# Optimization experiments

Hardware: AMD Instinct MI355X
Metric: run time of the kernel (lower is better)

## Reference

```python
import jax, jax.numpy as jnp
import numpy as np
from jax.ops import segment_sum, segment_max

N, F, H, HEADS, E, OUT = 50000, 256, 64, 4, 800000, 16


def setup_inputs() -> dict:
    key = jax.random.key(0)
    ks = jax.random.split(key, 16)
    s = 0.05
    return {
        "x": jax.random.normal(ks[0], (N, F), jnp.float32),
        "edge_index": jax.random.randint(ks[1], (2, E), 0, N, jnp.int64),
        # GCN layer params
        "W_gcn1": jax.random.normal(ks[2], (F, H), jnp.float32) * s,
        "b_gcn1": jnp.zeros((H,), jnp.float32),
        "W_gcn2": jax.random.normal(ks[3], (H, OUT), jnp.float32) * s,
        "b_gcn2": jnp.zeros((OUT,), jnp.float32),
        # GAT layer 1 (heads=HEADS, concat)
        "W_gat1": jax.random.normal(ks[4], (F, HEADS * H), jnp.float32) * s,
        "a_src1": jax.random.normal(ks[5], (HEADS, H), jnp.float32) * s,
        "a_dst1": jax.random.normal(ks[6], (HEADS, H), jnp.float32) * s,
        "b_gat1": jnp.zeros((HEADS * H,), jnp.float32),
        # GAT layer 2 (heads=1, concat=False)
        "W_gat2": jax.random.normal(ks[7], (HEADS * H, OUT), jnp.float32) * s,
        "a_src2": jax.random.normal(ks[8], (1, OUT), jnp.float32) * s,
        "a_dst2": jax.random.normal(ks[9], (1, OUT), jnp.float32) * s,
        "b_gat2": jnp.zeros((OUT,), jnp.float32),
    }


def _add_self_loops(edge_index, n):
    loop = jnp.arange(n, dtype=edge_index.dtype)
    src = jnp.concatenate([edge_index[0], loop])
    dst = jnp.concatenate([edge_index[1], loop])
    return src, dst


def _gcn(x, src, dst, norm, W, b, n):
    h = x @ W  # [N, out]
    out = segment_sum(h[src] * norm[:, None], dst, num_segments=n)
    return out + b


def _gat(x, src, dst, W, a_s, a_d, b, heads, concat, n):
    h = (x @ W).reshape(n, heads, -1)  # [N, heads, C]
    s_src = jnp.einsum("nhc,hc->nh", h, a_s)
    s_dst = jnp.einsum("nhc,hc->nh", h, a_d)
    e = jax.nn.leaky_relu(s_src[src] + s_dst[dst], 0.2)  # [Etot, heads]
    m = segment_max(e, dst, num_segments=n)               # per-dst softmax
    p = jnp.exp(e - m[dst])
    denom = segment_sum(p, dst, num_segments=n)
    alpha = p / denom[dst]
    out = segment_sum(h[src] * alpha[..., None], dst, num_segments=n)
    out = out.reshape(n, -1) if concat else out.mean(axis=1)
    return out + b


def reference(x, edge_index, W_gcn1, b_gcn1, W_gcn2, b_gcn2,
              W_gat1, a_src1, a_dst1, b_gat1,
              W_gat2, a_src2, a_dst2, b_gat2):
    n = x.shape[0]
    src, dst = _add_self_loops(edge_index, n)
    # symmetric GCN normalization on self-loop-augmented graph
    deg = segment_sum(jnp.ones_like(dst, x.dtype), dst, num_segments=n)
    dinv = jnp.where(deg > 0, jax.lax.rsqrt(deg), 0.0)
    norm = dinv[src] * dinv[dst]

    x_gcn = jax.nn.relu(_gcn(x, src, dst, norm, W_gcn1, b_gcn1, n))
    x_gcn = _gcn(x_gcn, src, dst, norm, W_gcn2, b_gcn2, n)

    x_gat = jax.nn.relu(_gat(x, src, dst, W_gat1, a_src1, a_dst1, b_gat1, HEADS, True, n))
    x_gat = _gat(x_gat, src, dst, W_gat2, a_src2, a_dst2, b_gat2, 1, False, n)

    return jnp.concatenate([x_gcn, x_gat], axis=1)
```

## Files before the change

### kernel.cpp

```cpp
#include <hip/hip_runtime.h>
#include <math.h>

#define NN     50000
#define FF     256
#define HH     64
#define NHEADS 4
#define EE     800000
#define OUTD   16

typedef __attribute__((ext_vector_type(8))) short short8;
typedef __attribute__((ext_vector_type(4))) float f32x4;

__device__ inline unsigned short f2bf(float f) {
    unsigned u = __builtin_bit_cast(unsigned, f);
    unsigned r = (u + 0x7fff + ((u >> 16) & 1)) >> 16;
    return (unsigned short)r;
}
__device__ inline float bf2f(unsigned short s) {
    unsigned u = ((unsigned)s) << 16;
    return __builtin_bit_cast(float, u);
}

__global__ void k_zero_int(int* __restrict__ p, int n) {
    int i = blockIdx.x * blockDim.x + threadIdx.x;
    if (i < n) p[i] = 0;
}

__global__ void k_count(const int* __restrict__ dst, int* __restrict__ cnt, int e) {
    int i = blockIdx.x * blockDim.x + threadIdx.x;
    if (i < e) atomicAdd(&cnt[dst[i]], 1);
}

__global__ __launch_bounds__(256) void k_scan_a(const int* __restrict__ cnt,
                                                int* __restrict__ partial, int n) {
    int i = blockIdx.x * 256 + threadIdx.x;
    int v = (i < n) ? cnt[i] : 0;
#pragma unroll
    for (int off = 32; off >= 1; off >>= 1) v += __shfl_xor(v, off, 64);
    __shared__ int ws[4];
    int wave = threadIdx.x >> 6;
    if ((threadIdx.x & 63) == 0) ws[wave] = v;
    __syncthreads();
    if (threadIdx.x == 0) partial[blockIdx.x] = ws[0] + ws[1] + ws[2] + ws[3];
}

__global__ __launch_bounds__(256) void k_scan_b(const int* __restrict__ partial,
                                                int* __restrict__ blockoff,
                                                int* __restrict__ total_out, int nb) {
    __shared__ int arr[256];
    int tid = threadIdx.x;
    arr[tid] = (tid < nb) ? partial[tid] : 0;
    __syncthreads();
#pragma unroll
    for (int off = 1; off < 256; off <<= 1) {
        int v = arr[tid];
        int add = (tid >= off) ? arr[tid - off] : 0;
        __syncthreads();
        arr[tid] = v + add;
        __syncthreads();
    }
    if (tid < nb) blockoff[tid] = arr[tid] - partial[tid];
    if (tid == 0) *total_out = arr[255];
}

__global__ __launch_bounds__(256) void k_scan_c(const int* __restrict__ cnt,
                                                const int* __restrict__ blockoff,
                                                int* __restrict__ row_start,
                                                int* __restrict__ cursor,
                                                float* __restrict__ dinv, int n) {
    __shared__ int arr[256];
    int tid = threadIdx.x;
    int i = blockIdx.x * 256 + tid;
    int c = (i < n) ? cnt[i] : 0;
    arr[tid] = c;
    __syncthreads();
#pragma unroll
    for (int off = 1; off < 256; off <<= 1) {
        int v = arr[tid];
        int add = (tid >= off) ? arr[tid - off] : 0;
        __syncthreads();
        arr[tid] = v + add;
        __syncthreads();
    }
    if (i < n) {
        int excl = arr[tid] - c + blockoff[blockIdx.x];
        row_start[i] = excl;
        cursor[i] = excl;
        dinv[i] = rsqrtf((float)(c + 1));
    }
}

__global__ void k_fill(const int* __restrict__ src, const int* __restrict__ dst,
                       int* __restrict__ cursor, int* __restrict__ col, int e) {
    int i = blockIdx.x * blockDim.x + threadIdx.x;
    if (i < e) {
        int d = dst[i];
        int pos = atomicAdd(&cursor[d], 1);
        col[pos] = src[i];
    }
}

template <int KB, int NT>
__global__ void k_pack_w(const float* __restrict__ W,
                         unsigned short* __restrict__ bhi,
                         unsigned short* __restrict__ blo) {
    int t_ = blockIdx.x * blockDim.x + threadIdx.x;
    const int total = KB * NT * 64;
    if (t_ >= total) return;
    int lane = t_ & 63;
    int tile = (t_ >> 6) % NT;
    int kb = (t_ >> 6) / NT;
    int q = lane >> 4, c = lane & 15;
    const int NC = NT * 16;
    size_t off = ((size_t)(kb * NT + tile) * 64 + lane) * 8;
#pragma unroll
    for (int j = 0; j < 8; j++) {
        float w = W[(size_t)(kb * 32 + q * 8 + j) * NC + tile * 16 + c];
        unsigned short h = f2bf(w);
        bhi[off + j] = h;
        blo[off + j] = f2bf(w - bf2f(h));
    }
}

template <int NT, bool SCALE, bool SCORES>
__global__ __launch_bounds__(256) void mfma_gemm(const float* __restrict__ A,
                                                 const unsigned short* __restrict__ Bhi,
                                                 const unsigned short* __restrict__ Blo,
                                                 unsigned short* __restrict__ Cbf,
                                                 const float* __restrict__ rowscale,
                                                 const float* __restrict__ a_s,
                                                 const float* __restrict__ a_d,
                                                 float* __restrict__ ssrc,
                                                 float* __restrict__ sdst,
                                                 int M) {
    const int K = 256, NC = NT * 16;
    __shared__ short8 bsh[NT * 64];
    __shared__ short8 bsl[NT * 64];
    int tid = threadIdx.x;
    int w = tid >> 6, lane = tid & 63, q = lane >> 4, c = lane & 15;
    int row_base = blockIdx.x * 64 + w * 16;
    int ar = min(row_base + c, M - 1);
    const float* ap = A + (size_t)ar * K + q * 8;

    f32x4 acc[NT];
#pragma unroll
    for (int t = 0; t < NT; t++) acc[t] = (f32x4){0.f, 0.f, 0.f, 0.f};

    for (int kb = 0; kb < 8; kb++) {
        float av[8];
        *(float4*)(av)     = *(const float4*)(ap + kb * 32);
        *(float4*)(av + 4) = *(const float4*)(ap + kb * 32 + 4);
        short8 ahi, alo;
#pragma unroll
        for (int j = 0; j < 8; j++) {
            unsigned short h = f2bf(av[j]);
            ahi[j] = (short)h;
            alo[j] = (short)f2bf(av[j] - bf2f(h));
        }
        const short8* gh = (const short8*)(Bhi + (size_t)kb * NT * 512);
        const short8* gl = (const short8*)(Blo + (size_t)kb * NT * 512);
        __syncthreads();
        for (int i = tid; i < NT * 64; i += 256) {
            bsh[i] = gh[i];
            bsl[i] = gl[i];
        }
        __syncthreads();
#pragma unroll
        for (int t = 0; t < NT; t++) {
            short8 bhi = bsh[t * 64 + lane];
            short8 blo = bsl[t * 64 + lane];
            acc[t] = __builtin_amdgcn_mfma_f32_16x16x32_bf16(ahi, bhi, acc[t], 0, 0, 0);
            acc[t] = __builtin_amdgcn_mfma_f32_16x16x32_bf16(alo, bhi, acc[t], 0, 0, 0);
            acc[t] = __builtin_amdgcn_mfma_f32_16x16x32_bf16(ahi, blo, acc[t], 0, 0, 0);
        }
    }

    if (SCORES) {
#pragma unroll
        for (int i = 0; i < 4; i++) {
            int r = row_base + q * 4 + i;
            float ss[4] = {0.f, 0.f, 0.f, 0.f};
            float sd[4] = {0.f, 0.f, 0.f, 0.f};
#pragma unroll
            for (int t = 0; t < NT; t++) {
                float v = acc[t][i];
                ss[t >> 2] += v * a_s[t * 16 + c];
                sd[t >> 2] += v * a_d[t * 16 + c];
            }
#pragma unroll
            for (int h = 0; h < 4; h++) {
#pragma unroll
                for (int off = 1; off <= 8; off <<= 1) {
                    ss[h] += __shfl_xor(ss[h], off, 16);
                    sd[h] += __shfl_xor(sd[h], off, 16);
                }
            }
            if (c == i && r < M) {
                *(float4*)(ssrc + (size_t)r * 4) = make_float4(ss[0], ss[1], ss[2], ss[3]);
                *(float4*)(sdst + (size_t)r * 4) = make_float4(sd[0], sd[1], sd[2], sd[3]);
            }
        }
    }

#pragma unroll
    for (int i = 0; i < 4; i++) {
        int r = row_base + q * 4 + i;
        if (r < M) {
            float sc = SCALE ? rowscale[r] : 1.0f;
#pragma unroll
            for (int t = 0; t < NT; t++)
                Cbf[(size_t)r * NC + t * 16 + c] = f2bf(acc[t][i] * sc);
        }
    }
}

template <int KB, bool SCALE, bool SC2>
__global__ __launch_bounds__(256) void mfma_n16(const unsigned short* __restrict__ A,
                                                const unsigned short* __restrict__ Bhi,
                                                const unsigned short* __restrict__ Blo,
                                                unsigned short* __restrict__ Cbf,
                                                const float* __restrict__ rowscale,
                                                const float* __restrict__ a_s2,
                                                const float* __restrict__ a_d2,
                                                float* __restrict__ s2s,
                                                float* __restrict__ s2d, int M) {
    const int K = KB * 32;
    int tid = threadIdx.x;
    int w = tid >> 6, lane = tid & 63, q = lane >> 4, c = lane & 15;
    int row_base = blockIdx.x * 64 + w * 16;
    int ar = min(row_base + c, M - 1);
    const unsigned short* ap = A + (size_t)ar * K + q * 8;
    f32x4 acc = (f32x4){0.f, 0.f, 0.f, 0.f};
#pragma unroll
    for (int kb = 0; kb < KB; kb++) {
        short8 av = *(const short8*)(ap + kb * 32);
        size_t bo = ((size_t)kb * 64 + lane) * 8;
        short8 bh = *(const short8*)(Bhi + bo);
        short8 bl = *(const short8*)(Blo + bo);
        acc = __builtin_amdgcn_mfma_f32_16x16x32_bf16(av, bh, acc, 0, 0, 0);
        acc = __builtin_amdgcn_mfma_f32_16x16x32_bf16(av, bl, acc, 0, 0, 0);
    }
    if (SC2) {
#pragma unroll
        for (int i = 0; i < 4; i++) {
            float ps = acc[i] * a_s2[c];
            float pd = acc[i] * a_d2[c];
#pragma unroll
            for (int off = 1; off <= 8; off <<= 1) {
                ps += __shfl_xor(ps, off, 16);
                pd += __shfl_xor(pd, off, 16);
            }
            int r = row_base + q * 4 + i;
            if (c == i && r < M) {
                s2s[r] = ps;
                s2d[r] = pd;
            }
        }
    }
#pragma unroll
    for (int i = 0; i < 4; i++) {
        int r = row_base + q * 4 + i;
        if (r < M) {
            float sc = SCALE ? rowscale[r] : 1.0f;
            Cbf[(size_t)r * 16 + c] = f2bf(acc[i] * sc);
        }
    }
}

__global__ __launch_bounds__(256) void gcn1_agg(const unsigned short* __restrict__ h,
                                                const int* __restrict__ rs,
                                                const int* __restrict__ col,
                                                const float* __restrict__ dinv,
                                                const float* __restrict__ b,
                                                unsigned short* __restrict__ out) {
    int wid = (blockIdx.x * 256 + threadIdx.x) >> 6;
    int lane = threadIdx.x & 63;
    if (wid >= NN) return;
    int g = lane >> 4;
    int cidx = (lane & 15) * 4;
    float di = dinv[wid];
    int beg = rs[wid], end = rs[wid + 1];
    float4 acc = make_float4(0.f, 0.f, 0.f, 0.f);

    for (int j0 = beg; j0 < end; j0 += 64) {
        int cnt = min(64, end - j0);
        int sreg = 0;
        if (lane < cnt) sreg = col[j0 + lane];
        for (int e = 0; e < cnt; e += 8) {
            int myE0 = e + g, myE1 = e + g + 4;
            int s0 = __shfl(sreg, myE0, 64);
            int s1 = __shfl(sreg, myE1, 64);
            ushort4 v0 = make_ushort4(0, 0, 0, 0), v1 = make_ushort4(0, 0, 0, 0);
            if (myE0 < cnt) v0 = *(const ushort4*)(h + (size_t)s0 * HH + cidx);
            if (myE1 < cnt) v1 = *(const ushort4*)(h + (size_t)s1 * HH + cidx);
            acc.x += bf2f(v0.x) + bf2f(v1.x);
            acc.y += bf2f(v0.y) + bf2f(v1.y);
            acc.z += bf2f(v0.z) + bf2f(v1.z);
            acc.w += bf2f(v0.w) + bf2f(v1.w);
        }
    }
#pragma unroll
    for (int off = 16; off <= 32; off <<= 1) {
        acc.x += __shfl_xor(acc.x, off, 64);
        acc.y += __shfl_xor(acc.y, off, 64);
        acc.z += __shfl_xor(acc.z, off, 64);
        acc.w += __shfl_xor(acc.w, off, 64);
    }
    if (g == 0) {
        ushort4 sv = *(const ushort4*)(h + (size_t)wid * HH + cidx);
        float4 bv = *(const float4*)(b + cidx);
        ushort4 o;
        o.x = f2bf(fmaxf((acc.x + bf2f(sv.x)) * di + bv.x, 0.f));
        o.y = f2bf(fmaxf((acc.y + bf2f(sv.y)) * di + bv.y, 0.f));
        o.z = f2bf(fmaxf((acc.z + bf2f(sv.z)) * di + bv.z, 0.f));
        o.w = f2bf(fmaxf((acc.w + bf2f(sv.w)) * di + bv.w, 0.f));
        *(ushort4*)(out + (size_t)wid * HH + cidx) = o;
    }
}

__global__ __launch_bounds__(256) void gat1_agg(const unsigned short* __restrict__ hg,
                                                const int* __restrict__ rs,
                                                const int* __restrict__ col,
                                                const float* __restrict__ ssrc,
                                                const float* __restrict__ sdst,
                                                const float* __restrict__ b,
                                                unsigned short* __restrict__ out) {
    __shared__ int s_lds[4][64];
    __shared__ float p_lds[4][64 * 4];
    int tid = threadIdx.x;
    int w = tid >> 6, lane = tid & 63;
    int wid = blockIdx.x * 4 + w;
    int hh = lane >> 4;
    int* sl = s_lds[w];
    float* pl = p_lds[w];

    float4 sd4 = *(const float4*)(sdst + (size_t)wid * 4);
    float sdv[4] = {sd4.x, sd4.y, sd4.z, sd4.w};
    float4 sf4 = *(const float4*)(ssrc + (size_t)wid * 4);
    float sfv[4] = {sf4.x, sf4.y, sf4.z, sf4.w};
    float psf[4];
#pragma unroll
    for (int h = 0; h < 4; h++) {
        float e = sfv[h] + sdv[h];
        e = (e >= 0.f) ? e : 0.2f * e;
        psf[h] = __expf(e);
    }
    float pse = (hh & 2) ? ((hh & 1) ? psf[3] : psf[2]) : ((hh & 1) ? psf[1] : psf[0]);
    const unsigned short* hbase = hg + lane * 4;
    ushort4 hvs = *(const ushort4*)(hbase + (size_t)wid * 256);
    float4 acc;
    acc.x = bf2f(hvs.x) * pse; acc.y = bf2f(hvs.y) * pse;
    acc.z = bf2f(hvs.z) * pse; acc.w = bf2f(hvs.w) * pse;

    float lsum[4] = {0.f, 0.f, 0.f, 0.f};
    int beg = rs[wid], end = rs[wid + 1];
    for (int j0 = beg; j0 < end; j0 += 64) {
        int cnt = min(64, end - j0);
        if (lane < cnt) {
            int sreg = col[j0 + lane];
            float4 sv = *(const float4*)(ssrc + (size_t)sreg * 4);
            float svv[4] = {sv.x, sv.y, sv.z, sv.w};
            float pv[4];
#pragma unroll
            for (int h = 0; h < 4; h++) {
                float e = svv[h] + sdv[h];
                e = (e >= 0.f) ? e : 0.2f * e;
                pv[h] = __expf(e);
                lsum[h] += pv[h];
            }
            sl[lane] = sreg;
            *(float4*)&pl[lane * 4] = make_float4(pv[0], pv[1], pv[2], pv[3]);
        }
        int e = 0;
        for (; e + 4 <= cnt; e += 4) {
            int s0 = sl[e], s1 = sl[e + 1], s2 = sl[e + 2], s3 = sl[e + 3];
            float p0 = pl[e * 4 + hh], p1 = pl[(e + 1) * 4 + hh];
            float p2 = pl[(e + 2) * 4 + hh], p3 = pl[(e + 3) * 4 + hh];
            ushort4 h0 = *(const ushort4*)(hbase + (size_t)s0 * 256);
            ushort4 h1 = *(const ushort4*)(hbase + (size_t)s1 * 256);
            ushort4 h2 = *(const ushort4*)(hbase + (size_t)s2 * 256);
            ushort4 h3 = *(const ushort4*)(hbase + (size_t)s3 * 256);
            acc.x += bf2f(h0.x) * p0; acc.y += bf2f(h0.y) * p0;
            acc.z += bf2f(h0.z) * p0; acc.w += bf2f(h0.w) * p0;
            acc.x += bf2f(h1.x) * p1; acc.y += bf2f(h1.y) * p1;
            acc.z += bf2f(h1.z) * p1; acc.w += bf2f(h1.w) * p1;
            acc.x += bf2f(h2.x) * p2; acc.y += bf2f(h2.y) * p2;
            acc.z += bf2f(h2.z) * p2; acc.w += bf2f(h2.w) * p2;
            acc.x += bf2f(h3.x) * p3; acc.y += bf2f(h3.y) * p3;
            acc.z += bf2f(h3.z) * p3; acc.w += bf2f(h3.w) * p3;
        }
        for (; e < cnt; e++) {
            int s = sl[e];
            float p = pl[e * 4 + hh];
            ushort4 hv = *(const ushort4*)(hbase + (size_t)s * 256);
            acc.x += bf2f(hv.x) * p; acc.y += bf2f(hv.y) * p;
            acc.z += bf2f(hv.z) * p; acc.w += bf2f(hv.w) * p;
        }
    }
#pragma unroll
    for (int h = 0; h < 4; h++) {
        float v = lsum[h];
        for (int off = 32; off >= 1; off >>= 1) v += __shfl_xor(v, off, 64);
        lsum[h] = v + psf[h];
    }
    float lt = (hh & 2) ? ((hh & 1) ? lsum[3] : lsum[2]) : ((hh & 1) ? lsum[1] : lsum[0]);
    float li = 1.0f / lt;
    float4 bv = *(const float4*)(b + lane * 4);
    ushort4 o;
    o.x = f2bf(fmaxf(acc.x * li + bv.x, 0.f));
    o.y = f2bf(fmaxf(acc.y * li + bv.y, 0.f));
    o.z = f2bf(fmaxf(acc.z * li + bv.z, 0.f));
    o.w = f2bf(fmaxf(acc.w * li + bv.w, 0.f));
    *(ushort4*)(out + (size_t)wid * 256 + lane * 4) = o;
}

__global__ __launch_bounds__(256) void final_agg(const unsigned short* __restrict__ h2,
                                                 const unsigned short* __restrict__ h2g,
                                                 const int* __restrict__ rs,
                                                 const int* __restrict__ col,
                                                 const float* __restrict__ dinv,
                                                 const float* __restrict__ s2s,
                                                 const float* __restrict__ s2d,
                                                 const float* __restrict__ bg2,
                                                 const float* __restrict__ bga2,
                                                 float* __restrict__ out) {
    int t = blockIdx.x * 256 + threadIdx.x;
    int node = t >> 4;
    int c = t & 15;
    float di = dinv[node];
    float sd = s2d[node];
    float es = s2s[node] + sd;
    es = (es >= 0.f) ? es : 0.2f * es;
    float psf = __expf(es);
    float accg = bf2f(h2[(size_t)node * 16 + c]);
    float acca = bf2f(h2g[(size_t)node * 16 + c]) * psf;
    float lp = 0.f;
    int beg = rs[node], end = rs[node + 1];
    for (int j0 = beg; j0 < end; j0 += 16) {
        int cnt = min(16, end - j0);
        int sreg = 0;
        float pr = 0.f;
        if (c < cnt) {
            sreg = col[j0 + c];
            float e = s2s[sreg] + sd;
            e = (e >= 0.f) ? e : 0.2f * e;
            pr = __expf(e);
            lp += pr;
        }
        for (int e = 0; e < cnt; e += 4) {
            int si[4];
            float pi[4];
#pragma unroll
            for (int u = 0; u < 4; u++) {
                si[u] = __shfl(sreg, (e + u) & 15, 16);
                pi[u] = __shfl(pr, (e + u) & 15, 16);
            }
            unsigned short g0[4], a0[4];
#pragma unroll
            for (int u = 0; u < 4; u++) {
                g0[u] = h2[(size_t)si[u] * 16 + c];
                a0[u] = h2g[(size_t)si[u] * 16 + c];
            }
#pragma unroll
            for (int u = 0; u < 4; u++) {
                if (e + u < cnt) {
                    accg += bf2f(g0[u]);
                    acca += bf2f(a0[u]) * pi[u];
                }
            }
        }
    }
    for (int off = 8; off >= 1; off >>= 1) lp += __shfl_xor(lp, off, 16);
    float l = lp + psf;
    out[(size_t)node * 32 + c] = accg * di + bg2[c];
    out[(size_t)node * 32 + 16 + c] = acca / l + bga2[c];
}

extern "C" void kernel_launch(void* const* d_in, const int* in_sizes, int n_in,
                              void* d_out, int out_size, void* d_ws, size_t ws_size,
                              hipStream_t stream) {
    const float* x      = (const float*)d_in[0];
    const int*   ei     = (const int*)d_in[1];
    const float* Wg1    = (const float*)d_in[2];
    const float* bg1    = (const float*)d_in[3];
    const float* Wg2    = (const float*)d_in[4];
    const float* bg2    = (const float*)d_in[5];
    const float* Wgat1  = (const float*)d_in[6];
    const float* a_src1 = (const float*)d_in[7];
    const float* a_dst1 = (const float*)d_in[8];
    const float* bgat1  = (const float*)d_in[9];
    const float* Wgat2  = (const float*)d_in[10];
    const float* a_src2 = (const float*)d_in[11];
    const float* a_dst2 = (const float*)d_in[12];
    const float* bgat2  = (const float*)d_in[13];
    float* out = (float*)d_out;

    const int* e_src = ei;
    const int* e_dst = ei + EE;

    char* wsb = (char*)d_ws;
    size_t o = 0;
    auto alloc = [&](size_t bytes) -> void* {
        void* p = wsb + o;
        o += (bytes + 255) & ~(size_t)255;
        return p;
    };
    float* dinv            = (float*)alloc(NN * 4);
    float* ssrc1           = (float*)alloc((size_t)NN * 16);
    float* sdst1           = (float*)alloc((size_t)NN * 16);
    unsigned short* h1b    = (unsigned short*)alloc((size_t)NN * HH * 2);
    unsigned short* xg1    = (unsigned short*)alloc((size_t)NN * HH * 2);
    unsigned short* h2b    = (unsigned short*)alloc((size_t)NN * 16 * 2);
    unsigned short* hgb    = (unsigned short*)alloc((size_t)NN * 256 * 2);
    unsigned short* xgat1  = (unsigned short*)alloc((size_t)NN * 256 * 2);
    unsigned short* h2gb   = (unsigned short*)alloc((size_t)NN * 16 * 2);
    float* s2src           = (float*)alloc(NN * 4);
    float* s2dst           = (float*)alloc(NN * 4);
    unsigned short* bhi1   = (unsigned short*)alloc(256 * 64 * 2);
    unsigned short* blo1   = (unsigned short*)alloc(256 * 64 * 2);
    unsigned short* bhi2   = (unsigned short*)alloc(256 * 256 * 2);
    unsigned short* blo2   = (unsigned short*)alloc(256 * 256 * 2);
    unsigned short* bhiG2  = (unsigned short*)alloc(64 * 16 * 2);
    unsigned short* bloG2  = (unsigned short*)alloc(64 * 16 * 2);
    unsigned short* bhiA2  = (unsigned short*)alloc(256 * 16 * 2);
    unsigned short* bloA2  = (unsigned short*)alloc(256 * 16 * 2);
    int* cnt               = (int*)alloc(NN * 4);
    int* rowstart          = (int*)alloc((NN + 1) * 4);
    int* cursor            = (int*)alloc(NN * 4);
    int* colarr            = (int*)alloc((size_t)EE * 4);
    int* partial           = (int*)alloc(256 * 4);
    int* blockoff          = (int*)alloc(256 * 4);

    const int TB = 256;
    const int NB = (NN + 255) / 256;
    k_zero_int<<<(NN + TB - 1) / TB, TB, 0, stream>>>(cnt, NN);
    k_count<<<(EE + TB - 1) / TB, TB, 0, stream>>>(e_dst, cnt, EE);
    k_scan_a<<<NB, TB, 0, stream>>>(cnt, partial, NN);
    k_scan_b<<<1, TB, 0, stream>>>(partial, blockoff, rowstart + NN, NB);
    k_scan_c<<<NB, TB, 0, stream>>>(cnt, blockoff, rowstart, cursor, dinv, NN);
    k_fill<<<(EE + TB - 1) / TB, TB, 0, stream>>>(e_src, e_dst, cursor, colarr, EE);
    k_pack_w<8, 4><<<(8 * 4 * 64 + TB - 1) / TB, TB, 0, stream>>>(Wg1, bhi1, blo1);
    k_pack_w<8, 16><<<(8 * 16 * 64 + TB - 1) / TB, TB, 0, stream>>>(Wgat1, bhi2, blo2);
    k_pack_w<2, 1><<<1, TB, 0, stream>>>(Wg2, bhiG2, bloG2);
    k_pack_w<8, 1><<<2, TB, 0, stream>>>(Wgat2, bhiA2, bloA2);

    const int GB = (NN + 63) / 64;
    const int G16 = (NN * 16) / 256;

    mfma_gemm<4, true, false><<<GB, TB, 0, stream>>>(x, bhi1, blo1, h1b, dinv,
                                                     nullptr, nullptr, nullptr, nullptr, NN);
    gcn1_agg<<<(NN * 64) / TB, TB, 0, stream>>>(h1b, rowstart, colarr, dinv, bg1, xg1);
    mfma_n16<2, true, false><<<GB, TB, 0, stream>>>(xg1, bhiG2, bloG2, h2b, dinv,
                                                    nullptr, nullptr, nullptr, nullptr, NN);

    mfma_gemm<16, false, true><<<GB, TB, 0, stream>>>(x, bhi2, blo2, hgb, nullptr,
                                                      a_src1, a_dst1, ssrc1, sdst1, NN);
    gat1_agg<<<NN / 4, TB, 0, stream>>>(hgb, rowstart, colarr, ssrc1, sdst1, bgat1, xgat1);
    mfma_n16<8, false, true><<<GB, TB, 0, stream>>>(xgat1, bhiA2, bloA2, h2gb, nullptr,
                                                    a_src2, a_dst2, s2src, s2dst, NN);

    final_agg<<<G16, TB, 0, stream>>>(h2b, h2gb, rowstart, colarr, dinv,
                                      s2src, s2dst, bg2, bgat2, out);
}
```

Measured before the change: 376.7 us.

## Process 128 rows per GEMM block, interleave final-layer features, unroll GCN gather

The x-projection GEMMs now compute two 64-row tiles per block, so each LDS-staged weight slab is reused across twice as many rows and the number of blocks is halved. The two 16-wide second-layer outputs (GCN and GAT) are written interleaved into one paired buffer. This lets final_agg fetch both with a single 32-bit gather per neighbour instead of two 16-bit gathers. The gcn1 aggregation loop processes 16 edges per iteration instead of 8 to keep more loads in flight. The costs are doubled accumulator registers in the GEMM (NT=16 means 128 accumulator floats), which may lower occupancy, and fewer blocks for 50000 rows.

```diff
diff --git a/kernel.cpp b/kernel.cpp
--- a/kernel.cpp
+++ b/kernel.cpp
@@ -138,24 +138,35 @@
     __shared__ short8 bsl[NT * 64];
     int tid = threadIdx.x;
     int w = tid >> 6, lane = tid & 63, q = lane >> 4, c = lane & 15;
-    int row_base = blockIdx.x * 64 + w * 16;
-    int ar = min(row_base + c, M - 1);
-    const float* ap = A + (size_t)ar * K + q * 8;
-
-    f32x4 acc[NT];
-#pragma unroll
-    for (int t = 0; t < NT; t++) acc[t] = (f32x4){0.f, 0.f, 0.f, 0.f};
+    int r0 = blockIdx.x * 128 + w * 16;
+    int r1 = r0 + 64;
+    int ar0 = min(r0 + c, M - 1);
+    int ar1 = min(r1 + c, M - 1);
+    const float* ap0 = A + (size_t)ar0 * K + q * 8;
+    const float* ap1 = A + (size_t)ar1 * K + q * 8;
+
+    f32x4 acc0[NT], acc1[NT];
+#pragma unroll
+    for (int t = 0; t < NT; t++) {
+        acc0[t] = (f32x4){0.f, 0.f, 0.f, 0.f};
+        acc1[t] = (f32x4){0.f, 0.f, 0.f, 0.f};
+    }
 
     for (int kb = 0; kb < 8; kb++) {
-        float av[8];
-        *(float4*)(av)     = *(const float4*)(ap + kb * 32);
-        *(float4*)(av + 4) = *(const float4*)(ap + kb * 32 + 4);
-        short8 ahi, alo;
+        float av0[8], av1[8];
+        *(float4*)(av0)     = *(const float4*)(ap0 + kb * 32);
+        *(float4*)(av0 + 4) = *(const float4*)(ap0 + kb * 32 + 4);
+        *(float4*)(av1)     = *(const float4*)(ap1 + kb * 32);
+        *(float4*)(av1 + 4) = *(const float4*)(ap1 + kb * 32 + 4);
+        short8 ahi0, alo0, ahi1, alo1;
 #pragma unroll
         for (int j = 0; j < 8; j++) {
-            unsigned short h = f2bf(av[j]);
-            ahi[j] = (short)h;
-            alo[j] = (short)f2bf(av[j] - bf2f(h));
+            unsigned short h0 = f2bf(av0[j]);
+            ahi0[j] = (short)h0;
+            alo0[j] = (short)f2bf(av0[j] - bf2f(h0));
+            unsigned short h1 = f2bf(av1[j]);
+            ahi1[j] = (short)h1;
+            alo1[j] = (short)f2bf(av1[j] - bf2f(h1));
         }
         const short8* gh = (const short8*)(Bhi + (size_t)kb * NT * 512);
         const short8* gl = (const short8*)(Blo + (size_t)kb * NT * 512);
@@ -169,21 +180,24 @@
         for (int t = 0; t < NT; t++) {
             short8 bhi = bsh[t * 64 + lane];
             short8 blo = bsl[t * 64 + lane];
-            acc[t] = __builtin_amdgcn_mfma_f32_16x16x32_bf16(ahi, bhi, acc[t], 0, 0, 0);
-            acc[t] = __builtin_amdgcn_mfma_f32_16x16x32_bf16(alo, bhi, acc[t], 0, 0, 0);
-            acc[t] = __builtin_amdgcn_mfma_f32_16x16x32_bf16(ahi, blo, acc[t], 0, 0, 0);
-        }
-    }
-
-    if (SCORES) {
+            acc0[t] = __builtin_amdgcn_mfma_f32_16x16x32_bf16(ahi0, bhi, acc0[t], 0, 0, 0);
+            acc0[t] = __builtin_amdgcn_mfma_f32_16x16x32_bf16(alo0, bhi, acc0[t], 0, 0, 0);
+            acc0[t] = __builtin_amdgcn_mfma_f32_16x16x32_bf16(ahi0, blo, acc0[t], 0, 0, 0);
+            acc1[t] = __builtin_amdgcn_mfma_f32_16x16x32_bf16(ahi1, bhi, acc1[t], 0, 0, 0);
+            acc1[t] = __builtin_amdgcn_mfma_f32_16x16x32_bf16(alo1, bhi, acc1[t], 0, 0, 0);
+            acc1[t] = __builtin_amdgcn_mfma_f32_16x16x32_bf16(ahi1, blo, acc1[t], 0, 0, 0);
+        }
+    }
+
+    auto do_scores = [&](const f32x4 (&ac)[NT], int rbase) {
 #pragma unroll
         for (int i = 0; i < 4; i++) {
-            int r = row_base + q * 4 + i;
+            int r = rbase + q * 4 + i;
             float ss[4] = {0.f, 0.f, 0.f, 0.f};
             float sd[4] = {0.f, 0.f, 0.f, 0.f};
 #pragma unroll
             for (int t = 0; t < NT; t++) {
-                float v = acc[t][i];
+                float v = ac[t][i];
                 ss[t >> 2] += v * a_s[t * 16 + c];
                 sd[t >> 2] += v * a_d[t * 16 + c];
             }
@@ -200,21 +214,29 @@
                 *(float4*)(sdst + (size_t)r * 4) = make_float4(sd[0], sd[1], sd[2], sd[3]);
             }
         }
-    }
-
-#pragma unroll
-    for (int i = 0; i < 4; i++) {
-        int r = row_base + q * 4 + i;
-        if (r < M) {
-            float sc = SCALE ? rowscale[r] : 1.0f;
-#pragma unroll
-            for (int t = 0; t < NT; t++)
-                Cbf[(size_t)r * NC + t * 16 + c] = f2bf(acc[t][i] * sc);
-        }
-    }
-}
-
-template <int KB, bool SCALE, bool SC2>
+    };
+    if (SCORES) {
+        do_scores(acc0, r0);
+        do_scores(acc1, r1);
+    }
+
+    auto do_store = [&](const f32x4 (&ac)[NT], int rbase) {
+#pragma unroll
+        for (int i = 0; i < 4; i++) {
+            int r = rbase + q * 4 + i;
+            if (r < M) {
+                float sc = SCALE ? rowscale[r] : 1.0f;
+#pragma unroll
+                for (int t = 0; t < NT; t++)
+                    Cbf[(size_t)r * NC + t * 16 + c] = f2bf(ac[t][i] * sc);
+            }
+        }
+    };
+    do_store(acc0, r0);
+    do_store(acc1, r1);
+}
+
+template <int KB, bool SCALE, bool SC2, int OFS>
 __global__ __launch_bounds__(256) void mfma_n16(const unsigned short* __restrict__ A,
                                                 const unsigned short* __restrict__ Bhi,
                                                 const unsigned short* __restrict__ Blo,
@@ -262,7 +284,7 @@
         int r = row_base + q * 4 + i;
         if (r < M) {
             float sc = SCALE ? rowscale[r] : 1.0f;
-            Cbf[(size_t)r * 16 + c] = f2bf(acc[i] * sc);
+            Cbf[((size_t)r * 16 + c) * 2 + OFS] = f2bf(acc[i] * sc);
         }
     }
 }
@@ -286,17 +308,22 @@
         int cnt = min(64, end - j0);
         int sreg = 0;
         if (lane < cnt) sreg = col[j0 + lane];
-        for (int e = 0; e < cnt; e += 8) {
-            int myE0 = e + g, myE1 = e + g + 4;
-            int s0 = __shfl(sreg, myE0, 64);
-            int s1 = __shfl(sreg, myE1, 64);
+        for (int e = 0; e < cnt; e += 16) {
+            int m0 = e + g, m1 = e + g + 4, m2 = e + g + 8, m3 = e + g + 12;
+            int s0 = __shfl(sreg, m0, 64);
+            int s1 = __shfl(sreg, m1, 64);
+            int s2 = __shfl(sreg, m2, 64);
+            int s3 = __shfl(sreg, m3, 64);
             ushort4 v0 = make_ushort4(0, 0, 0, 0), v1 = make_ushort4(0, 0, 0, 0);
-            if (myE0 < cnt) v0 = *(const ushort4*)(h + (size_t)s0 * HH + cidx);
-            if (myE1 < cnt) v1 = *(const ushort4*)(h + (size_t)s1 * HH + cidx);
-            acc.x += bf2f(v0.x) + bf2f(v1.x);
-            acc.y += bf2f(v0.y) + bf2f(v1.y);
-            acc.z += bf2f(v0.z) + bf2f(v1.z);
-            acc.w += bf2f(v0.w) + bf2f(v1.w);
+            ushort4 v2 = make_ushort4(0, 0, 0, 0), v3 = make_ushort4(0, 0, 0, 0);
+            if (m0 < cnt) v0 = *(const ushort4*)(h + (size_t)s0 * HH + cidx);
+            if (m1 < cnt) v1 = *(const ushort4*)(h + (size_t)s1 * HH + cidx);
+            if (m2 < cnt) v2 = *(const ushort4*)(h + (size_t)s2 * HH + cidx);
+            if (m3 < cnt) v3 = *(const ushort4*)(h + (size_t)s3 * HH + cidx);
+            acc.x += (bf2f(v0.x) + bf2f(v1.x)) + (bf2f(v2.x) + bf2f(v3.x));
+            acc.y += (bf2f(v0.y) + bf2f(v1.y)) + (bf2f(v2.y) + bf2f(v3.y));
+            acc.z += (bf2f(v0.z) + bf2f(v1.z)) + (bf2f(v2.z) + bf2f(v3.z));
+            acc.w += (bf2f(v0.w) + bf2f(v1.w)) + (bf2f(v2.w) + bf2f(v3.w));
         }
     }
 #pragma unroll
@@ -414,8 +441,7 @@
     *(ushort4*)(out + (size_t)wid * 256 + lane * 4) = o;
 }
 
-__global__ __launch_bounds__(256) void final_agg(const unsigned short* __restrict__ h2,
-                                                 const unsigned short* __restrict__ h2g,
+__global__ __launch_bounds__(256) void final_agg(const unsigned* __restrict__ hp,
                                                  const int* __restrict__ rs,
                                                  const int* __restrict__ col,
                                                  const float* __restrict__ dinv,
@@ -432,8 +458,9 @@
     float es = s2s[node] + sd;
     es = (es >= 0.f) ? es : 0.2f * es;
     float psf = __expf(es);
-    float accg = bf2f(h2[(size_t)node * 16 + c]);
-    float acca = bf2f(h2g[(size_t)node * 16 + c]) * psf;
+    unsigned pvs = hp[(size_t)node * 16 + c];
+    float accg = bf2f((unsigned short)pvs);
+    float acca = bf2f((unsigned short)(pvs >> 16)) * psf;
     float lp = 0.f;
     int beg = rs[node], end = rs[node + 1];
     for (int j0 = beg; j0 < end; j0 += 16) {
@@ -455,17 +482,14 @@
                 si[u] = __shfl(sreg, (e + u) & 15, 16);
                 pi[u] = __shfl(pr, (e + u) & 15, 16);
             }
-            unsigned short g0[4], a0[4];
-#pragma unroll
-            for (int u = 0; u < 4; u++) {
-                g0[u] = h2[(size_t)si[u] * 16 + c];
-                a0[u] = h2g[(size_t)si[u] * 16 + c];
-            }
+            unsigned hv[4];
+#pragma unroll
+            for (int u = 0; u < 4; u++) hv[u] = hp[(size_t)si[u] * 16 + c];
 #pragma unroll
             for (int u = 0; u < 4; u++) {
                 if (e + u < cnt) {
-                    accg += bf2f(g0[u]);
-                    acca += bf2f(a0[u]) * pi[u];
+                    accg += bf2f((unsigned short)hv[u]);
+                    acca += bf2f((unsigned short)(hv[u] >> 16)) * pi[u];
                 }
             }
         }
@@ -510,10 +534,9 @@
     float* sdst1           = (float*)alloc((size_t)NN * 16);
     unsigned short* h1b    = (unsigned short*)alloc((size_t)NN * HH * 2);
     unsigned short* xg1    = (unsigned short*)alloc((size_t)NN * HH * 2);
-    unsigned short* h2b    = (unsigned short*)alloc((size_t)NN * 16 * 2);
     unsigned short* hgb    = (unsigned short*)alloc((size_t)NN * 256 * 2);
     unsigned short* xgat1  = (unsigned short*)alloc((size_t)NN * 256 * 2);
-    unsigned short* h2gb   = (unsigned short*)alloc((size_t)NN * 16 * 2);
+    unsigned short* pairb  = (unsigned short*)alloc((size_t)NN * 16 * 4);
     float* s2src           = (float*)alloc(NN * 4);
     float* s2dst           = (float*)alloc(NN * 4);
     unsigned short* bhi1   = (unsigned short*)alloc(256 * 64 * 2);
@@ -544,21 +567,22 @@
     k_pack_w<2, 1><<<1, TB, 0, stream>>>(Wg2, bhiG2, bloG2);
     k_pack_w<8, 1><<<2, TB, 0, stream>>>(Wgat2, bhiA2, bloA2);
 
+    const int GB128 = (NN + 127) / 128;
     const int GB = (NN + 63) / 64;
     const int G16 = (NN * 16) / 256;
 
-    mfma_gemm<4, true, false><<<GB, TB, 0, stream>>>(x, bhi1, blo1, h1b, dinv,
-                                                     nullptr, nullptr, nullptr, nullptr, NN);
+    mfma_gemm<4, true, false><<<GB128, TB, 0, stream>>>(x, bhi1, blo1, h1b, dinv,
+                                                        nullptr, nullptr, nullptr, nullptr, NN);
     gcn1_agg<<<(NN * 64) / TB, TB, 0, stream>>>(h1b, rowstart, colarr, dinv, bg1, xg1);
-    mfma_n16<2, true, false><<<GB, TB, 0, stream>>>(xg1, bhiG2, bloG2, h2b, dinv,
-                                                    nullptr, nullptr, nullptr, nullptr, NN);
-
-    mfma_gemm<16, false, true><<<GB, TB, 0, stream>>>(x, bhi2, blo2, hgb, nullptr,
-                                                      a_src1, a_dst1, ssrc1, sdst1, NN);
+    mfma_n16<2, true, false, 0><<<GB, TB, 0, stream>>>(xg1, bhiG2, bloG2, pairb, dinv,
+                                                       nullptr, nullptr, nullptr, nullptr, NN);
+
+    mfma_gemm<16, false, true><<<GB128, TB, 0, stream>>>(x, bhi2, blo2, hgb, nullptr,
+                                                         a_src1, a_dst1, ssrc1, sdst1, NN);
     gat1_agg<<<NN / 4, TB, 0, stream>>>(hgb, rowstart, colarr, ssrc1, sdst1, bgat1, xgat1);
-    mfma_n16<8, false, true><<<GB, TB, 0, stream>>>(xgat1, bhiA2, bloA2, h2gb, nullptr,
-                                                    a_src2, a_dst2, s2src, s2dst, NN);
-
-    final_agg<<<G16, TB, 0, stream>>>(h2b, h2gb, rowstart, colarr, dinv,
+    mfma_n16<8, false, true, 1><<<GB, TB, 0, stream>>>(xgat1, bhiA2, bloA2, pairb, nullptr,
+                                                       a_src2, a_dst2, s2src, s2dst, NN);
+
+    final_agg<<<G16, TB, 0, stream>>>((const unsigned*)pairb, rowstart, colarr, dinv,
                                       s2src, s2dst, bg2, bgat2, out);
 }
```

Result: slower. 389.5 us (+3.4%).
